# Kernel tuning notes

Hardware: AMD Instinct MI355X
Metric: run time of the kernel (lower is better)

Reference implementation:

```python
import jax, jax.numpy as jnp
import numpy as np

B, C, H, W = 512, 256, 7, 7
NS, HS, WS = 16, 14, 14
CK = 128            # key/value channels of the 1x1 convs
REP = 1024          # MLP_HEAD_DIM
IN = 2 * CK * H * W # 12544 = concat(query_value, attended_value) flattened


def setup_inputs() -> dict:
    key = jax.random.key(0)
    ks = jax.random.split(key, 14)
    s = lambda n: 1.0 / np.sqrt(n)
    f32 = jnp.float32
    return {
        "x": jax.random.normal(ks[0], (B, C, H, W), f32),
        "sup_features": jax.random.normal(ks[1], (NS, C, HS, WS), f32),
        # 1x1 conv weights [out_c, in_c] + biases
        "Wqv": jax.random.normal(ks[2], (CK, C), f32) * s(C),
        "bqv": jnp.zeros((CK,), f32),
        "Wqk": jax.random.normal(ks[3], (CK, C), f32) * s(C),
        "bqk": jnp.zeros((CK,), f32),
        "Wsv": jax.random.normal(ks[4], (CK, C), f32) * s(C),
        "bsv": jnp.zeros((CK,), f32),
        "Wsk": jax.random.normal(ks[5], (CK, C), f32) * s(C),
        "bsk": jnp.zeros((CK,), f32),
        # fc layers, torch Linear convention: W [out, in]
        "W6c": jax.random.normal(ks[6], (REP, IN), f32) * s(IN),
        "b6c": jnp.zeros((REP,), f32),
        "W7c": jax.random.normal(ks[7], (REP, REP), f32) * s(REP),
        "b7c": jnp.zeros((REP,), f32),
        "W6r": jax.random.normal(ks[8], (REP, IN), f32) * s(IN),
        "b6r": jnp.zeros((REP,), f32),
        "W7r": jax.random.normal(ks[9], (REP, REP), f32) * s(REP),
        "b7r": jnp.zeros((REP,), f32),
    }


def _conv1x1(w, b, t):
    # 1x1 conv == per-pixel channel mixing
    return jnp.einsum('oc,bchw->bohw', w, t) + b[None, :, None, None]


def reference(x, sup_features, Wqv, bqv, Wqk, bqk, Wsv, bsv, Wsk, bsk,
              W6c, b6c, W7c, b7c, W6r, b6r, W7r, b7r):
    qv = _conv1x1(Wqv, bqv, x)                                          # [B,128,H,W]
    qk = _conv1x1(Wqk, bqk, x).transpose(0, 2, 3, 1).reshape(-1, CK)    # [B*H*W,128]
    sv = _conv1x1(Wsv, bsv, sup_features).transpose(0, 2, 3, 1).reshape(-1, CK)  # [M,128]
    sk = _conv1x1(Wsk, bsk, sup_features).transpose(1, 0, 2, 3).reshape(CK, -1)  # [128,M]
    sim = jax.nn.softmax(qk @ sk, axis=-1)                              # [B*H*W, M] (unscaled, as in source)
    att = (sim @ sv).reshape(B, H, W, CK).transpose(0, 3, 1, 2)         # [B,128,H,W]
    fuse = jnp.concatenate([qv, att], axis=1).reshape(B, -1)            # [B,12544]
    xr = jax.nn.relu(fuse @ W6r.T + b6r)
    xr = jax.nn.relu(xr @ W7r.T + b7r)
    xc = jax.nn.relu(fuse @ W6c.T + b6c)
    xc = jax.nn.relu(xc @ W7c.T + b7c)
    return (xc, xr)
```

## Files before the change

### kernel.cpp

```cpp
#include <hip/hip_runtime.h>
#include <hip/hip_bf16.h>
#include <stdint.h>

typedef short short8 __attribute__((ext_vector_type(8)));
typedef float f32x4 __attribute__((ext_vector_type(4)));
typedef ushort ushort4v __attribute__((ext_vector_type(4)));

#define M_Q   25088
#define M_S   3136
#define IN_   12544
#define LOG2E  1.44269504f
#define SHIFT2 57.7078016f
#define NZ    8
#define FZ    8
#define KSTR  136
#define PSTR  40
#define WSTR  40

__device__ __forceinline__ ushort f2bf(float f) {
  union { float f; uint32_t u; } v; v.f = f;
  uint32_t r = v.u + 0x7fffu + ((v.u >> 16) & 1u);
  return (ushort)(r >> 16);
}
__device__ __forceinline__ ushort f2bf_fast(float f) {
  union { float f; uint32_t u; } v; v.f = f;
  return (ushort)((v.u + 0x8000u) >> 16);
}
__device__ __forceinline__ float bf2f(ushort u) {
  union { uint32_t u; float f; } v; v.u = ((uint32_t)u) << 16;
  return v.f;
}
__device__ __forceinline__ f32x4 mfma16(short8 a, short8 b, f32x4 c) {
  return __builtin_amdgcn_mfma_f32_16x16x32_bf16(a, b, c, 0, 0, 0);
}

__global__ __launch_bounds__(256) void pack_all(
    const float* __restrict__ W6c, const float* __restrict__ W6r,
    ushort* __restrict__ W6p,
    const float* __restrict__ W7c, const float* __restrict__ W7r,
    ushort* __restrict__ W7p,
    const float* __restrict__ Wqv, const float* __restrict__ Wqk,
    const float* __restrict__ bqv, const float* __restrict__ bqk,
    const float* __restrict__ Wsv, const float* __restrict__ Wsk,
    const float* __restrict__ bsv, const float* __restrict__ bsk,
    ushort* __restrict__ Wq_h, float* __restrict__ biasq,
    ushort* __restrict__ Ws_h, float* __restrict__ biass) {
  __shared__ ushort tile[IN_];
  const int bid = blockIdx.x;
  if (bid < 2048) {
    const int n = bid;
    const float* src = (n < 1024) ? (W6c + (size_t)n * IN_)
                                  : (W6r + (size_t)(n - 1024) * IN_);
    ushort* dst = W6p + (size_t)n * IN_;
#pragma unroll 7
    for (int j = 0; j < 49; ++j) {
      int i = j * 256 + threadIdx.x;
      tile[i] = f2bf(src[i]);
    }
    __syncthreads();
#pragma unroll 7
    for (int j = 0; j < 49; ++j) {
      int o = j * 256 + threadIdx.x;
      int c = o & 255, p = o >> 8;
      dst[o] = tile[c * 49 + p];
    }
  } else if (bid < 10240) {
    int idx = (bid - 2048) * 256 + threadIdx.x;
    float v = (idx < 1048576) ? W7c[idx] : W7r[idx - 1048576];
    W7p[idx] = f2bf(v);
  } else {
    int idx = (bid - 10240) * 256 + threadIdx.x;
    if (idx < 65536) {
      int n = idx >> 8;
      const float* W = (n < 128) ? (Wqv + n * 256) : (Wqk + (n - 128) * 256);
      Wq_h[idx] = f2bf(W[idx & 255]);
    } else if (idx < 131072) {
      int j = idx - 65536;
      int n = j >> 8;
      const float* W = (n < 128) ? (Wsv + n * 256) : (Wsk + (n - 128) * 256);
      Ws_h[j] = f2bf(W[j & 255]);
    } else if (idx < 131328) {
      int n = idx - 131072;
      biasq[n] = (n < 128) ? bqv[n] : bqk[n - 128];
    } else if (idx < 131584) {
      int n = idx - 131328;
      biass[n] = (n < 128) ? bsv[n] : bsk[n - 128];
    }
  }
}

__global__ __launch_bounds__(256) void gemm_conv_q(
    const float* __restrict__ x, const ushort* __restrict__ Bh,
    const float* __restrict__ bias, ushort* __restrict__ fuse,
    ushort* __restrict__ qk_h) {
  const int lane = threadIdx.x & 63, wv = threadIdx.x >> 6;
  const int r = lane & 15, g = lane >> 4;
  const int row0 = blockIdx.x * 64 + wv * 16;
  const int q = row0 + r;
  const int b = q / 49, p = q - b * 49;
  const float* xb = x + (size_t)b * IN_ + p;
  f32x4 acc[16];
#pragma unroll
  for (int i = 0; i < 16; ++i) acc[i] = f32x4{0.f, 0.f, 0.f, 0.f};
#pragma unroll
  for (int kc = 0; kc < 8; ++kc) {
    const float* s = xb + (size_t)(kc * 32 + g * 8) * 49;
    short8 ah;
#pragma unroll
    for (int j = 0; j < 8; ++j) ah[j] = (short)f2bf(s[(size_t)j * 49]);
    const ushort* bbh = Bh + r * 256 + kc * 32 + g * 8;
#pragma unroll
    for (int nt = 0; nt < 16; ++nt) {
      short8 bh = *(const short8*)(bbh + nt * 16 * 256);
      acc[nt] = mfma16(ah, bh, acc[nt]);
    }
  }
  const int qr = row0 + g * 4;
#pragma unroll
  for (int nt = 0; nt < 16; ++nt) {
    int n = nt * 16 + r;
    float bs = bias[n];
#pragma unroll
    for (int e = 0; e < 4; ++e) {
      float v = acc[nt][e] + bs;
      int qq = qr + e;
      if (nt < 8) {
        int bb = qq / 49, pp = qq - bb * 49;
        fuse[(size_t)bb * IN_ + pp * 256 + n] = f2bf(v);
      } else {
        qk_h[(size_t)qq * 128 + (n - 128)] = f2bf(v * LOG2E);
      }
    }
  }
}

__global__ __launch_bounds__(256) void gemm_conv_s(
    const float* __restrict__ sup, const ushort* __restrict__ Bh,
    const float* __restrict__ bias, ushort* __restrict__ svT,
    ushort* __restrict__ sk_h) {
  const int lane = threadIdx.x & 63, wv = threadIdx.x >> 6;
  const int r = lane & 15, g = lane >> 4;
  const int row0 = blockIdx.x * 64 + wv * 16;
  const int nb = blockIdx.y;
  const int q = row0 + r;
  const int b = q / 196, p = q - b * 196;
  const float* xb = sup + (size_t)b * 256 * 196 + p;
  f32x4 acc[8];
#pragma unroll
  for (int i = 0; i < 8; ++i) acc[i] = f32x4{0.f, 0.f, 0.f, 0.f};
#pragma unroll
  for (int kc = 0; kc < 8; ++kc) {
    const float* s = xb + (size_t)(kc * 32 + g * 8) * 196;
    short8 ah;
#pragma unroll
    for (int j = 0; j < 8; ++j) ah[j] = (short)f2bf(s[(size_t)j * 196]);
    const ushort* bbh = Bh + (size_t)(nb * 128 + r) * 256 + kc * 32 + g * 8;
#pragma unroll
    for (int nt = 0; nt < 8; ++nt) {
      short8 bh = *(const short8*)(bbh + nt * 16 * 256);
      acc[nt] = mfma16(ah, bh, acc[nt]);
    }
  }
  const int qr = row0 + g * 4;
#pragma unroll
  for (int nt = 0; nt < 8; ++nt) {
    int nl = nt * 16 + r;
    float bs = bias[nb * 128 + nl];
#pragma unroll
    for (int e = 0; e < 4; ++e) {
      float v = acc[nt][e] + bs;
      int k = qr + e;
      if (nb == 0) {
        svT[(size_t)nl * M_S + k] = f2bf(v);
      } else {
        sk_h[(size_t)k * 128 + nl] = f2bf(v);
      }
    }
  }
}

#define LOAD_TILE(T)                                                            \
  do {                                                                          \
    const int kb_ = (T) * 32;                                                   \
    pkh0 = *(const short8*)(Kh + (size_t)(kb_ + row0s) * 128 + c8s * 8);        \
    pkh1 = *(const short8*)(Kh + (size_t)(kb_ + row0s + 16) * 128 + c8s * 8);   \
    pv0  = *(const short8*)(Vt + (size_t)cvs * M_S + kb_ + kc2s * 8);           \
    pv1  = *(const short8*)(Vt + (size_t)(cvs + 64) * M_S + kb_ + kc2s * 8);    \
  } while (0)
#define PUBLISH(B)                                                              \
  do {                                                                          \
    *(short8*)(&khs[B][kloff0]) = pkh0;                                         \
    *(short8*)(&khs[B][kloff1]) = pkh1;                                         \
    *(short8*)(&vvs[B][voff0]) = pv0;                                           \
    *(short8*)(&vvs[B][voff1]) = pv1;                                           \
  } while (0)

__global__ __launch_bounds__(256) void attn_kernel(
    const ushort* __restrict__ Qh, const ushort* __restrict__ Kh,
    const ushort* __restrict__ Vt, ushort* __restrict__ pnum,
    float* __restrict__ pden) {
  __shared__ ushort khs[2][32 * KSTR];
  __shared__ ushort vvs[2][128 * 32];
  __shared__ ushort plds[4][16 * PSTR];
  const int tid = threadIdx.x;
  const int w = tid >> 6, lane = tid & 63;
  const int r = lane & 15, g = lane >> 4;
  const int q0 = blockIdx.x * 128 + w * 32;
  const int z = blockIdx.y;
  const int t0 = z * 12 + (z < 2 ? z : 2);
  const int tn = 12 + (z < 2 ? 1 : 0);
  ushort* pw = plds[w];

  const int row0s = tid >> 4, c8s = tid & 15;
  const int cvs = tid >> 2, kc2s = tid & 3;
  const int kloff0 = row0s * KSTR + c8s * 8;
  const int kloff1 = (row0s + 16) * KSTR + c8s * 8;
  const int voff0 = cvs * 32 + kc2s * 8;
  const int voff1 = (cvs + 64) * 32 + kc2s * 8;

  short8 aq[2][4];
#pragma unroll
  for (int mt = 0; mt < 2; ++mt)
#pragma unroll
    for (int kc = 0; kc < 4; ++kc)
      aq[mt][kc] = *(const short8*)(Qh + (size_t)(q0 + mt * 16 + r) * 128 + kc * 32 + g * 8);

  f32x4 acc[2][8];
#pragma unroll
  for (int mt = 0; mt < 2; ++mt)
#pragma unroll
    for (int ct = 0; ct < 8; ++ct) acc[mt][ct] = f32x4{0.f, 0.f, 0.f, 0.f};
  float den[2][4];
#pragma unroll
  for (int mt = 0; mt < 2; ++mt)
#pragma unroll
    for (int e = 0; e < 4; ++e) den[mt][e] = 0.f;

  short8 pkh0, pkh1, pv0, pv1;
  LOAD_TILE(t0);
  PUBLISH(0);
  if (tn > 1) LOAD_TILE(t0 + 1);
  __syncthreads();

  for (int i = 0; i < tn; ++i) {
    const int b = i & 1;
    if (i + 1 < tn) {
      PUBLISH(b ^ 1);
      if (i + 2 < tn) LOAD_TILE(t0 + i + 2);
    }
    f32x4 lg[2][2];
    __builtin_amdgcn_s_setprio(1);
#pragma unroll
    for (int kt = 0; kt < 2; ++kt) {
      const int kbase = (kt * 16 + r) * KSTR;
      short8 bh[4];
#pragma unroll
      for (int kc = 0; kc < 4; ++kc)
        bh[kc] = *(const short8*)(&khs[b][kbase + (kc * 4 + g) * 8]);
#pragma unroll
      for (int mt = 0; mt < 2; ++mt) {
        f32x4 c = f32x4{0.f, 0.f, 0.f, 0.f};
#pragma unroll
        for (int kc = 0; kc < 4; ++kc)
          c = mfma16(aq[mt][kc], bh[kc], c);
        lg[mt][kt] = c;
      }
    }
    __builtin_amdgcn_s_setprio(0);
    short8 vf[8];
#pragma unroll
    for (int ct = 0; ct < 8; ++ct)
      vf[ct] = *(const short8*)(&vvs[b][(ct * 16 + r) * 32 + g * 8]);
#pragma unroll
    for (int mt = 0; mt < 2; ++mt) {
#pragma unroll
      for (int kt = 0; kt < 2; ++kt)
#pragma unroll
        for (int e = 0; e < 4; ++e) {
          float p = __builtin_amdgcn_exp2f(lg[mt][kt][e] - SHIFT2);
          den[mt][e] += p;
          pw[(g * 4 + e) * PSTR + kt * 16 + r] = f2bf_fast(p);
        }
      short8 pf = *(const short8*)(pw + r * PSTR + g * 8);
      __builtin_amdgcn_s_setprio(1);
#pragma unroll
      for (int ct = 0; ct < 8; ++ct)
        acc[mt][ct] = mfma16(pf, vf[ct], acc[mt][ct]);
      __builtin_amdgcn_s_setprio(0);
    }
    __syncthreads();
  }

#pragma unroll
  for (int mt = 0; mt < 2; ++mt)
#pragma unroll
    for (int e = 0; e < 4; ++e) {
      float d = den[mt][e];
      d += __shfl_xor(d, 1);
      d += __shfl_xor(d, 2);
      d += __shfl_xor(d, 4);
      d += __shfl_xor(d, 8);
      den[mt][e] = d;
    }
#pragma unroll
  for (int mt = 0; mt < 2; ++mt)
#pragma unroll
    for (int ct = 0; ct < 8; ++ct)
#pragma unroll
      for (int e = 0; e < 4; ++e) {
        int q = q0 + mt * 16 + g * 4 + e;
        int c = ct * 16 + r;
        pnum[((size_t)z * M_Q + q) * 128 + c] = f2bf_fast(acc[mt][ct][e]);
      }
  if (r == 0) {
#pragma unroll
    for (int mt = 0; mt < 2; ++mt)
#pragma unroll
      for (int e = 0; e < 4; ++e)
        pden[(size_t)z * M_Q + q0 + mt * 16 + g * 4 + e] = den[mt][e];
  }
}

__global__ void attn_reduce(const ushort* __restrict__ pnum, const float* __restrict__ pden,
                            ushort* __restrict__ fuse) {
  int idx = blockIdx.x * 256 + threadIdx.x;
  int q = idx >> 5;
  int c4 = (idx & 31) * 4;
  float4 s = {0.f, 0.f, 0.f, 0.f};
  float d = 0.f;
#pragma unroll
  for (int z = 0; z < NZ; ++z) {
    ushort4v v = *(const ushort4v*)(pnum + ((size_t)z * M_Q + q) * 128 + c4);
    s.x += bf2f(v[0]); s.y += bf2f(v[1]); s.z += bf2f(v[2]); s.w += bf2f(v[3]);
    d += pden[(size_t)z * M_Q + q];
  }
  float inv = 1.0f / d;
  int b = q / 49, p = q - b * 49;
  ushort4v o;
  o[0] = f2bf(s.x * inv); o[1] = f2bf(s.y * inv);
  o[2] = f2bf(s.z * inv); o[3] = f2bf(s.w * inv);
  *(ushort4v*)(fuse + (size_t)b * IN_ + p * 256 + 128 + c4) = o;
}

__global__ __launch_bounds__(512) void fc6_kernel(
    const ushort* __restrict__ fuse, const ushort* __restrict__ W6p,
    float* __restrict__ part) {
  __shared__ ushort wlds[2][64 * WSTR];
  const int lane = threadIdx.x & 63, wv = threadIdx.x >> 6;
  const int r = lane & 15, g = lane >> 4;
  const int m0 = wv * 64;
  const int kz = blockIdx.x & 7;
  const int nidx = (blockIdx.x >> 3) + 4 * blockIdx.y;
  const int n0 = nidx * 64;
  const int k0 = kz * 1568;

  const int srow = threadIdx.x >> 2;
  const int skc  = (threadIdx.x & 3) * 8;
  const bool stager = (threadIdx.x < 256);
  const size_t wgbase = (size_t)(n0 + (srow & 63)) * IN_ + k0 + skc;
  const int wloff = (srow & 63) * WSTR + skc;

  f32x4 acc[4][4];
#pragma unroll
  for (int mt = 0; mt < 4; ++mt)
#pragma unroll
    for (int nt = 0; nt < 4; ++nt) acc[mt][nt] = f32x4{0.f, 0.f, 0.f, 0.f};

  short8 rA, rB;
  if (stager) {
    rA = *(const short8*)(W6p + wgbase);
    *(short8*)(&wlds[0][wloff]) = rA;
    rA = *(const short8*)(W6p + wgbase + 32);
    rB = *(const short8*)(W6p + wgbase + 64);
  }
  __syncthreads();

  for (int t = 0; t < 49; ++t) {
    const int b = t & 1;
    if (t + 1 < 49 && stager) {
      *(short8*)(&wlds[b ^ 1][wloff]) = rA;
      rA = rB;
      if (t + 3 < 49) rB = *(const short8*)(W6p + wgbase + (size_t)(t + 3) * 32);
    }
    const int kcol = k0 + t * 32 + g * 8;
    short8 af[4];
#pragma unroll
    for (int mt = 0; mt < 4; ++mt)
      af[mt] = *(const short8*)(fuse + (size_t)(m0 + mt * 16 + r) * IN_ + kcol);
    short8 bfr[4];
#pragma unroll
    for (int nt = 0; nt < 4; ++nt)
      bfr[nt] = *(const short8*)(&wlds[b][(nt * 16 + r) * WSTR + g * 8]);
#pragma unroll
    for (int mt = 0; mt < 4; ++mt)
#pragma unroll
      for (int nt = 0; nt < 4; ++nt) acc[mt][nt] = mfma16(af[mt], bfr[nt], acc[mt][nt]);
    __syncthreads();
  }
#pragma unroll
  for (int mt = 0; mt < 4; ++mt)
#pragma unroll
    for (int nt = 0; nt < 4; ++nt)
#pragma unroll
      for (int e = 0; e < 4; ++e) {
        int m = m0 + mt * 16 + g * 4 + e;
        int n = n0 + nt * 16 + r;
        part[(size_t)kz * 1048576 + (size_t)m * 2048 + n] = acc[mt][nt][e];
      }
}

__global__ void fc6_reduce(const float* __restrict__ part, const float* __restrict__ b6c,
                           const float* __restrict__ b6r, ushort* __restrict__ X7) {
  int idx = blockIdx.x * 256 + threadIdx.x;
  int n = idx & 2047;
  float s = 0.f;
#pragma unroll
  for (int z = 0; z < FZ; ++z) s += part[(size_t)z * 1048576 + idx];
  s += (n < 1024) ? b6c[n] : b6r[n - 1024];
  s = fmaxf(s, 0.f);
  X7[idx] = f2bf(s);
}

__global__ __launch_bounds__(128) void fc7_kernel(
    const ushort* __restrict__ X7, const ushort* __restrict__ W7p,
    const float* __restrict__ b7c, const float* __restrict__ b7r,
    float* __restrict__ out) {
  const int lane = threadIdx.x & 63, wv = threadIdx.x >> 6;
  const int r = lane & 15, g = lane >> 4;
  const int m0 = blockIdx.x * 32 + wv * 16;
  const int n0 = blockIdx.y * 32;
  const int half = (n0 >= 1024) ? 1 : 0;
  const int nn0 = n0 - half * 1024;
  const float* b7 = half ? b7r : b7c;
  f32x4 acc[2];
#pragma unroll
  for (int nt = 0; nt < 2; ++nt) acc[nt] = f32x4{0.f, 0.f, 0.f, 0.f};
  const ushort* arow = X7 + (size_t)(m0 + r) * 2048 + half * 1024;
  for (int kk = 0; kk < 1024; kk += 32) {
    short8 a = *(const short8*)(arow + kk + g * 8);
#pragma unroll
    for (int nt = 0; nt < 2; ++nt) {
      short8 bb = *(const short8*)(W7p + (size_t)(half * 1024 + nn0 + nt * 16 + r) * 1024 + kk + g * 8);
      acc[nt] = mfma16(a, bb, acc[nt]);
    }
  }
  float* obase = out + (size_t)half * 524288;
#pragma unroll
  for (int nt = 0; nt < 2; ++nt) {
#pragma unroll
    for (int e = 0; e < 4; ++e) {
      int m = m0 + g * 4 + e;
      int n = nn0 + nt * 16 + r;
      obase[(size_t)m * 1024 + n] = fmaxf(acc[nt][e] + b7[n], 0.f);
    }
  }
}

extern "C" void kernel_launch(void* const* d_in, const int* in_sizes, int n_in,
                              void* d_out, int out_size, void* d_ws, size_t ws_size,
                              hipStream_t stream) {
  const float* x    = (const float*)d_in[0];
  const float* sup  = (const float*)d_in[1];
  const float* Wqv  = (const float*)d_in[2];
  const float* bqv  = (const float*)d_in[3];
  const float* Wqk  = (const float*)d_in[4];
  const float* bqk  = (const float*)d_in[5];
  const float* Wsv  = (const float*)d_in[6];
  const float* bsv  = (const float*)d_in[7];
  const float* Wsk  = (const float*)d_in[8];
  const float* bsk  = (const float*)d_in[9];
  const float* W6c  = (const float*)d_in[10];
  const float* b6c  = (const float*)d_in[11];
  const float* W7c  = (const float*)d_in[12];
  const float* b7c  = (const float*)d_in[13];
  const float* W6r  = (const float*)d_in[14];
  const float* b6r  = (const float*)d_in[15];
  const float* W7r  = (const float*)d_in[16];
  const float* b7r  = (const float*)d_in[17];
  float* out = (float*)d_out;

  char* base = (char*)d_ws;
  size_t off = 0;
  auto alloc = [&](size_t bytes) {
    char* p = base + off;
    off += (bytes + 255) & ~(size_t)255;
    return p;
  };
  char* regionB = alloc((size_t)NZ * M_Q * 128 * 2);
  ushort* pnum = (ushort*)regionB;
  float*  part = (float*)regionB;
  ushort* W6p  = (ushort*)alloc((size_t)2048 * IN_ * 2);
  ushort* W7p  = (ushort*)alloc((size_t)2048 * 1024 * 2);
  ushort* Wq_h = (ushort*)alloc(65536 * 2);
  ushort* Ws_h = (ushort*)alloc(65536 * 2);
  float*  biasq = (float*)alloc(256 * 4);
  float*  biass = (float*)alloc(256 * 4);
  ushort* fuse = (ushort*)alloc((size_t)512 * IN_ * 2);
  ushort* qk_h = (ushort*)alloc((size_t)M_Q * 128 * 2);
  ushort* sk_h = (ushort*)alloc((size_t)M_S * 128 * 2);
  ushort* svT  = (ushort*)alloc((size_t)M_S * 128 * 2);
  float*  pden = (float*)alloc((size_t)NZ * M_Q * 4);
  ushort* X7   = (ushort*)alloc((size_t)512 * 2048 * 2);
  if (off > ws_size) return;

  pack_all<<<dim3(10755), dim3(256), 0, stream>>>(W6c, W6r, W6p, W7c, W7r, W7p,
                                                  Wqv, Wqk, bqv, bqk, Wsv, Wsk,
                                                  bsv, bsk, Wq_h, biasq, Ws_h, biass);
  gemm_conv_q<<<dim3(392), dim3(256), 0, stream>>>(x, Wq_h, biasq, fuse, qk_h);
  gemm_conv_s<<<dim3(49, 2), dim3(256), 0, stream>>>(sup, Ws_h, biass, svT, sk_h);
  attn_kernel<<<dim3(196, NZ), dim3(256), 0, stream>>>(qk_h, sk_h, svT, pnum, pden);
  attn_reduce<<<dim3(3136), dim3(256), 0, stream>>>(pnum, pden, fuse);
  fc6_kernel<<<dim3(32, FZ), dim3(512), 0, stream>>>(fuse, W6p, part);
  fc6_reduce<<<dim3(4096), dim3(256), 0, stream>>>(part, b6c, b6r, X7);
  fc7_kernel<<<dim3(16, 64), dim3(128), 0, stream>>>(X7, W7p, b7c, b7r, out);
}
```

Baseline: 252.1 us.

## Overlap fc weight packing with attention and merge the two conv GEMM kernels

The large fc6/fc7 weight conversion moves out of the first kernel and into the attention launch as extra blocks, so its memory-bound bf16 packing can run alongside the compute-bound attention blocks. The query and support 1x1 conv GEMMs are merged into one launch using a block-index split, and only the small conv weights are still packed up front. This cuts launches and hides packing traffic. The cost is that the attention kernel now reserves a shared-memory buffer big enough for either role, which may lower occupancy, and block scheduling order decides how much actually overlaps.

```diff
diff --git a/kernel.cpp b/kernel.cpp
--- a/kernel.cpp
+++ b/kernel.cpp
@@ -16,6 +16,7 @@
 #define KSTR  136
 #define PSTR  40
 #define WSTR  40
+#define NATT  1568
 
 __device__ __forceinline__ ushort f2bf(float f) {
   union { float f; uint32_t u; } v; v.f = f;
@@ -34,146 +35,114 @@
   return __builtin_amdgcn_mfma_f32_16x16x32_bf16(a, b, c, 0, 0, 0);
 }
 
-__global__ __launch_bounds__(256) void pack_all(
-    const float* __restrict__ W6c, const float* __restrict__ W6r,
-    ushort* __restrict__ W6p,
-    const float* __restrict__ W7c, const float* __restrict__ W7r,
-    ushort* __restrict__ W7p,
-    const float* __restrict__ Wqv, const float* __restrict__ Wqk,
-    const float* __restrict__ bqv, const float* __restrict__ bqk,
-    const float* __restrict__ Wsv, const float* __restrict__ Wsk,
-    const float* __restrict__ bsv, const float* __restrict__ bsk,
-    ushort* __restrict__ Wq_h, float* __restrict__ biasq,
-    ushort* __restrict__ Ws_h, float* __restrict__ biass) {
-  __shared__ ushort tile[IN_];
-  const int bid = blockIdx.x;
-  if (bid < 2048) {
-    const int n = bid;
-    const float* src = (n < 1024) ? (W6c + (size_t)n * IN_)
-                                  : (W6r + (size_t)(n - 1024) * IN_);
-    ushort* dst = W6p + (size_t)n * IN_;
-#pragma unroll 7
-    for (int j = 0; j < 49; ++j) {
-      int i = j * 256 + threadIdx.x;
-      tile[i] = f2bf(src[i]);
-    }
-    __syncthreads();
-#pragma unroll 7
-    for (int j = 0; j < 49; ++j) {
-      int o = j * 256 + threadIdx.x;
-      int c = o & 255, p = o >> 8;
-      dst[o] = tile[c * 49 + p];
-    }
-  } else if (bid < 10240) {
-    int idx = (bid - 2048) * 256 + threadIdx.x;
-    float v = (idx < 1048576) ? W7c[idx] : W7r[idx - 1048576];
-    W7p[idx] = f2bf(v);
-  } else {
-    int idx = (bid - 10240) * 256 + threadIdx.x;
-    if (idx < 65536) {
-      int n = idx >> 8;
-      const float* W = (n < 128) ? (Wqv + n * 256) : (Wqk + (n - 128) * 256);
-      Wq_h[idx] = f2bf(W[idx & 255]);
-    } else if (idx < 131072) {
-      int j = idx - 65536;
-      int n = j >> 8;
-      const float* W = (n < 128) ? (Wsv + n * 256) : (Wsk + (n - 128) * 256);
-      Ws_h[j] = f2bf(W[j & 255]);
-    } else if (idx < 131328) {
-      int n = idx - 131072;
-      biasq[n] = (n < 128) ? bqv[n] : bqk[n - 128];
-    } else if (idx < 131584) {
-      int n = idx - 131328;
-      biass[n] = (n < 128) ? bsv[n] : bsk[n - 128];
-    }
-  }
-}
-
-__global__ __launch_bounds__(256) void gemm_conv_q(
-    const float* __restrict__ x, const ushort* __restrict__ Bh,
-    const float* __restrict__ bias, ushort* __restrict__ fuse,
-    ushort* __restrict__ qk_h) {
+__global__ void pack_w(const float* __restrict__ Wqv, const float* __restrict__ Wqk,
+                       const float* __restrict__ bqv, const float* __restrict__ bqk,
+                       const float* __restrict__ Wsv, const float* __restrict__ Wsk,
+                       const float* __restrict__ bsv, const float* __restrict__ bsk,
+                       ushort* __restrict__ Wq_h, float* __restrict__ biasq,
+                       ushort* __restrict__ Ws_h, float* __restrict__ biass) {
+  int idx = blockIdx.x * 256 + threadIdx.x;
+  if (idx < 65536) {
+    int n = idx >> 8;
+    const float* W = (n < 128) ? (Wqv + n * 256) : (Wqk + (n - 128) * 256);
+    Wq_h[idx] = f2bf(W[idx & 255]);
+  } else if (idx < 131072) {
+    int j = idx - 65536;
+    int n = j >> 8;
+    const float* W = (n < 128) ? (Wsv + n * 256) : (Wsk + (n - 128) * 256);
+    Ws_h[j] = f2bf(W[j & 255]);
+  } else if (idx < 131328) {
+    int n = idx - 131072;
+    biasq[n] = (n < 128) ? bqv[n] : bqk[n - 128];
+  } else if (idx < 131584) {
+    int n = idx - 131328;
+    biass[n] = (n < 128) ? bsv[n] : bsk[n - 128];
+  }
+}
+
+__global__ __launch_bounds__(256) void gemm_conv(
+    const float* __restrict__ x, const float* __restrict__ sup,
+    const ushort* __restrict__ Wq_h, const ushort* __restrict__ Ws_h,
+    const float* __restrict__ biasq, const float* __restrict__ biass,
+    ushort* __restrict__ fuse, ushort* __restrict__ qk_h,
+    ushort* __restrict__ svT, ushort* __restrict__ sk_h) {
   const int lane = threadIdx.x & 63, wv = threadIdx.x >> 6;
   const int r = lane & 15, g = lane >> 4;
-  const int row0 = blockIdx.x * 64 + wv * 16;
-  const int q = row0 + r;
-  const int b = q / 49, p = q - b * 49;
-  const float* xb = x + (size_t)b * IN_ + p;
-  f32x4 acc[16];
-#pragma unroll
-  for (int i = 0; i < 16; ++i) acc[i] = f32x4{0.f, 0.f, 0.f, 0.f};
-#pragma unroll
-  for (int kc = 0; kc < 8; ++kc) {
-    const float* s = xb + (size_t)(kc * 32 + g * 8) * 49;
-    short8 ah;
-#pragma unroll
-    for (int j = 0; j < 8; ++j) ah[j] = (short)f2bf(s[(size_t)j * 49]);
-    const ushort* bbh = Bh + r * 256 + kc * 32 + g * 8;
+  if (blockIdx.x < 392) {
+    const int row0 = blockIdx.x * 64 + wv * 16;
+    const int q = row0 + r;
+    const int b = q / 49, p = q - b * 49;
+    const float* xb = x + (size_t)b * IN_ + p;
+    f32x4 acc[16];
+#pragma unroll
+    for (int i = 0; i < 16; ++i) acc[i] = f32x4{0.f, 0.f, 0.f, 0.f};
+#pragma unroll
+    for (int kc = 0; kc < 8; ++kc) {
+      const float* s = xb + (size_t)(kc * 32 + g * 8) * 49;
+      short8 ah;
+#pragma unroll
+      for (int j = 0; j < 8; ++j) ah[j] = (short)f2bf(s[(size_t)j * 49]);
+      const ushort* bbh = Wq_h + r * 256 + kc * 32 + g * 8;
+#pragma unroll
+      for (int nt = 0; nt < 16; ++nt) {
+        short8 bh = *(const short8*)(bbh + nt * 16 * 256);
+        acc[nt] = mfma16(ah, bh, acc[nt]);
+      }
+    }
+    const int qr = row0 + g * 4;
 #pragma unroll
     for (int nt = 0; nt < 16; ++nt) {
-      short8 bh = *(const short8*)(bbh + nt * 16 * 256);
-      acc[nt] = mfma16(ah, bh, acc[nt]);
-    }
-  }
-  const int qr = row0 + g * 4;
-#pragma unroll
-  for (int nt = 0; nt < 16; ++nt) {
-    int n = nt * 16 + r;
-    float bs = bias[n];
-#pragma unroll
-    for (int e = 0; e < 4; ++e) {
-      float v = acc[nt][e] + bs;
-      int qq = qr + e;
-      if (nt < 8) {
-        int bb = qq / 49, pp = qq - bb * 49;
-        fuse[(size_t)bb * IN_ + pp * 256 + n] = f2bf(v);
-      } else {
-        qk_h[(size_t)qq * 128 + (n - 128)] = f2bf(v * LOG2E);
-      }
-    }
-  }
-}
-
-__global__ __launch_bounds__(256) void gemm_conv_s(
-    const float* __restrict__ sup, const ushort* __restrict__ Bh,
-    const float* __restrict__ bias, ushort* __restrict__ svT,
-    ushort* __restrict__ sk_h) {
-  const int lane = threadIdx.x & 63, wv = threadIdx.x >> 6;
-  const int r = lane & 15, g = lane >> 4;
-  const int row0 = blockIdx.x * 64 + wv * 16;
-  const int nb = blockIdx.y;
-  const int q = row0 + r;
-  const int b = q / 196, p = q - b * 196;
-  const float* xb = sup + (size_t)b * 256 * 196 + p;
-  f32x4 acc[8];
-#pragma unroll
-  for (int i = 0; i < 8; ++i) acc[i] = f32x4{0.f, 0.f, 0.f, 0.f};
-#pragma unroll
-  for (int kc = 0; kc < 8; ++kc) {
-    const float* s = xb + (size_t)(kc * 32 + g * 8) * 196;
-    short8 ah;
-#pragma unroll
-    for (int j = 0; j < 8; ++j) ah[j] = (short)f2bf(s[(size_t)j * 196]);
-    const ushort* bbh = Bh + (size_t)(nb * 128 + r) * 256 + kc * 32 + g * 8;
+      int n = nt * 16 + r;
+      float bs = biasq[n];
+#pragma unroll
+      for (int e = 0; e < 4; ++e) {
+        float v = acc[nt][e] + bs;
+        int qq = qr + e;
+        if (nt < 8) {
+          int bb = qq / 49, pp = qq - bb * 49;
+          fuse[(size_t)bb * IN_ + pp * 256 + n] = f2bf(v);
+        } else {
+          qk_h[(size_t)qq * 128 + (n - 128)] = f2bf(v * LOG2E);
+        }
+      }
+    }
+  } else {
+    const int sb = blockIdx.x - 392;
+    const int nb = sb / 49;
+    const int row0 = (sb - nb * 49) * 64 + wv * 16;
+    const int q = row0 + r;
+    const int b = q / 196, p = q - b * 196;
+    const float* xb = sup + (size_t)b * 256 * 196 + p;
+    f32x4 acc[8];
+#pragma unroll
+    for (int i = 0; i < 8; ++i) acc[i] = f32x4{0.f, 0.f, 0.f, 0.f};
+#pragma unroll
+    for (int kc = 0; kc < 8; ++kc) {
+      const float* s = xb + (size_t)(kc * 32 + g * 8) * 196;
+      short8 ah;
+#pragma unroll
+      for (int j = 0; j < 8; ++j) ah[j] = (short)f2bf(s[(size_t)j * 196]);
+      const ushort* bbh = Ws_h + (size_t)(nb * 128 + r) * 256 + kc * 32 + g * 8;
+#pragma unroll
+      for (int nt = 0; nt < 8; ++nt) {
+        short8 bh = *(const short8*)(bbh + nt * 16 * 256);
+        acc[nt] = mfma16(ah, bh, acc[nt]);
+      }
+    }
+    const int qr = row0 + g * 4;
 #pragma unroll
     for (int nt = 0; nt < 8; ++nt) {
-      short8 bh = *(const short8*)(bbh + nt * 16 * 256);
-      acc[nt] = mfma16(ah, bh, acc[nt]);
-    }
-  }
-  const int qr = row0 + g * 4;
-#pragma unroll
-  for (int nt = 0; nt < 8; ++nt) {
-    int nl = nt * 16 + r;
-    float bs = bias[nb * 128 + nl];
-#pragma unroll
-    for (int e = 0; e < 4; ++e) {
-      float v = acc[nt][e] + bs;
-      int k = qr + e;
-      if (nb == 0) {
-        svT[(size_t)nl * M_S + k] = f2bf(v);
-      } else {
-        sk_h[(size_t)k * 128 + nl] = f2bf(v);
+      int nl = nt * 16 + r;
+      float bs = biass[nb * 128 + nl];
+#pragma unroll
+      for (int e = 0; e < 4; ++e) {
+        float v = acc[nt][e] + bs;
+        int k = qr + e;
+        if (nb == 0) {
+          svT[(size_t)nl * M_S + k] = f2bf(v);
+        } else {
+          sk_h[(size_t)k * 128 + nl] = f2bf(v);
+        }
       }
     }
   }
@@ -195,18 +164,55 @@
     *(short8*)(&vvs[B][voff1]) = pv1;                                           \
   } while (0)
 
-__global__ __launch_bounds__(256) void attn_kernel(
+__global__ __launch_bounds__(256) void attn_pack_kernel(
     const ushort* __restrict__ Qh, const ushort* __restrict__ Kh,
     const ushort* __restrict__ Vt, ushort* __restrict__ pnum,
-    float* __restrict__ pden) {
-  __shared__ ushort khs[2][32 * KSTR];
-  __shared__ ushort vvs[2][128 * 32];
-  __shared__ ushort plds[4][16 * PSTR];
+    float* __restrict__ pden,
+    const float* __restrict__ W6c, const float* __restrict__ W6r,
+    ushort* __restrict__ W6p,
+    const float* __restrict__ W7c, const float* __restrict__ W7r,
+    ushort* __restrict__ W7p) {
+  __shared__ char smem[38912];
+  const int bid = blockIdx.x;
   const int tid = threadIdx.x;
+
+  if (bid >= NATT) {
+    const int pb = bid - NATT;
+    if (pb < 2048) {
+      ushort* tile = (ushort*)smem;
+      const int n = pb;
+      const float* src = (n < 1024) ? (W6c + (size_t)n * IN_)
+                                    : (W6r + (size_t)(n - 1024) * IN_);
+      ushort* dst = W6p + (size_t)n * IN_;
+#pragma unroll 7
+      for (int j = 0; j < 49; ++j) {
+        int i = j * 256 + tid;
+        tile[i] = f2bf(src[i]);
+      }
+      __syncthreads();
+#pragma unroll 7
+      for (int j = 0; j < 49; ++j) {
+        int o = j * 256 + tid;
+        int c = o & 255, p = o >> 8;
+        dst[o] = tile[c * 49 + p];
+      }
+    } else {
+      int idx = (pb - 2048) * 256 + tid;
+      float v = (idx < 1048576) ? W7c[idx] : W7r[idx - 1048576];
+      W7p[idx] = f2bf(v);
+    }
+    return;
+  }
+
+  ushort (*khs)[32 * KSTR]  = (ushort(*)[32 * KSTR])smem;
+  ushort (*vvs)[128 * 32]   = (ushort(*)[128 * 32])(smem + 17408);
+  ushort (*plds)[16 * PSTR] = (ushort(*)[16 * PSTR])(smem + 33792);
+
+  const int z = bid / 196;
+  const int bx = bid - z * 196;
   const int w = tid >> 6, lane = tid & 63;
   const int r = lane & 15, g = lane >> 4;
-  const int q0 = blockIdx.x * 128 + w * 32;
-  const int z = blockIdx.y;
+  const int q0 = bx * 128 + w * 32;
   const int t0 = z * 12 + (z < 2 ? z : 2);
   const int tn = 12 + (z < 2 ? 1 : 0);
   ushort* pw = plds[w];
@@ -503,12 +509,12 @@
   ushort* X7   = (ushort*)alloc((size_t)512 * 2048 * 2);
   if (off > ws_size) return;
 
-  pack_all<<<dim3(10755), dim3(256), 0, stream>>>(W6c, W6r, W6p, W7c, W7r, W7p,
-                                                  Wqv, Wqk, bqv, bqk, Wsv, Wsk,
-                                                  bsv, bsk, Wq_h, biasq, Ws_h, biass);
-  gemm_conv_q<<<dim3(392), dim3(256), 0, stream>>>(x, Wq_h, biasq, fuse, qk_h);
-  gemm_conv_s<<<dim3(49, 2), dim3(256), 0, stream>>>(sup, Ws_h, biass, svT, sk_h);
-  attn_kernel<<<dim3(196, NZ), dim3(256), 0, stream>>>(qk_h, sk_h, svT, pnum, pden);
+  pack_w<<<dim3(515), dim3(256), 0, stream>>>(Wqv, Wqk, bqv, bqk, Wsv, Wsk, bsv, bsk,
+                                              Wq_h, biasq, Ws_h, biass);
+  gemm_conv<<<dim3(490), dim3(256), 0, stream>>>(x, sup, Wq_h, Ws_h, biasq, biass,
+                                                 fuse, qk_h, svT, sk_h);
+  attn_pack_kernel<<<dim3(NATT + 2048 + 8192), dim3(256), 0, stream>>>(
+      qk_h, sk_h, svT, pnum, pden, W6c, W6r, W6p, W7c, W7r, W7p);
   attn_reduce<<<dim3(3136), dim3(256), 0, stream>>>(pnum, pden, fuse);
   fc6_kernel<<<dim3(32, FZ), dim3(512), 0, stream>>>(fuse, W6p, part);
   fc6_reduce<<<dim3(4096), dim3(256), 0, stream>>>(part, b6c, b6r, X7);
```

New measurement: 241.9 us. -4.1%, faster.
